# Optimization experiments

Hardware: AMD Instinct MI355X
Metric: run time of the kernel (lower is better)

## Reference

```python
import jax, jax.numpy as jnp
import numpy as np

N = 50000      # nodes
E = 500000     # edges per adjacency (avg degree ~10)
IN = 128       # in_dim == hidden_dim so layer weights stack cleanly
HID = 128
C = 40         # n_classes
L = 3          # n_layers
DEG = 10.0


def setup_inputs() -> dict:
    key = jax.random.key(0)
    ks = jax.random.split(key, 14)
    x0 = jax.random.normal(ks[0], (N, IN), jnp.float32)
    # COO sparse adjacency (row-sorted for efficient segment_sum); values mimic mean-normalized weights
    adj_row = jnp.sort(jax.random.randint(ks[1], (E,), 0, N, jnp.int32))
    adj_col = jax.random.randint(ks[2], (E,), 0, N, jnp.int32)
    adj_val = jax.random.uniform(ks[3], (E,), jnp.float32) / DEG
    adj_b_row = jnp.sort(jax.random.randint(ks[4], (E,), 0, N, jnp.int32))
    adj_b_col = jax.random.randint(ks[5], (E,), 0, N, jnp.int32)
    adj_b_val = jax.random.uniform(ks[6], (E,), jnp.float32) / DEG
    id_old_value_new = jax.random.randint(ks[7], (N,), 0, N, jnp.int32)
    mix_ratio = jnp.array([0.5], jnp.float32)
    s = 1.0 / np.sqrt(HID)
    # SAGEConv params: lin_l (applied to aggregated neighbors, carries bias) and lin_r (root)
    Wl = jax.random.uniform(ks[8], (L, HID, HID), jnp.float32, -s, s)
    Wr = jax.random.uniform(ks[9], (L, HID, HID), jnp.float32, -s, s)
    b_sage = jax.random.uniform(ks[10], (L, HID), jnp.float32, -s, s)
    so = 1.0 / np.sqrt(HID)
    W_out = jax.random.uniform(ks[11], (HID, C), jnp.float32, -so, so)
    b_out = jax.random.uniform(ks[12], (C,), jnp.float32, -so, so)
    return dict(x0=x0, adj_row=adj_row, adj_col=adj_col, adj_val=adj_val,
                adj_b_row=adj_b_row, adj_b_col=adj_b_col, adj_b_val=adj_b_val,
                mix_ratio=mix_ratio, id_old_value_new=id_old_value_new,
                Wl=Wl, Wr=Wr, b_sage=b_sage, W_out=W_out, b_out=b_out)


def _sage(x_src, x_dst, row, col, val, Wl_i, Wr_i, b_i):
    # spmm: aggr = adj @ x_src  (gather neighbor feats, scale by edge value, scatter-add to rows)
    msg = x_src[col] * val[:, None]                       # [E, HID]
    aggr = jax.ops.segment_sum(msg, row, num_segments=N)  # [N, HID]
    return aggr @ Wl_i + x_dst @ Wr_i + b_i


def reference(x0, adj_row, adj_col, adj_val, adj_b_row, adj_b_col, adj_b_val,
              mix_ratio, id_old_value_new, Wl, Wr, b_sage, W_out, b_out):
    r = mix_ratio
    # Branch A pre-aggregation stack (dropout is identity in eval mode)
    aggr_xs = [x0]
    x = x0
    for i in range(L - 1):
        x = jax.nn.relu(_sage(x, x, adj_row, adj_col, adj_val, Wl[i], Wr[i], b_sage[i]))
        aggr_xs.append(x)
    # Branch B: gather-based re-indexing of branch-A features
    aggr_xs_b = [h[id_old_value_new] for h in aggr_xs]
    x_mix = aggr_xs[0] * r + aggr_xs_b[0] * (1.0 - r)
    for i in range(L):
        x_new = jax.nn.relu(_sage(aggr_xs[i], x_mix, adj_row, adj_col, adj_val, Wl[i], Wr[i], b_sage[i]))
        x_new_b = jax.nn.relu(_sage(aggr_xs_b[i], x_mix, adj_b_row, adj_b_col, adj_b_val, Wl[i], Wr[i], b_sage[i]))
        x_mix = x_new * r + x_new_b * (1.0 - r)
    logits = x_mix @ W_out + b_out
    return jax.nn.log_softmax(logits, axis=-1)
```

## Files before the change

kernel.cpp:

```cpp
#include <hip/hip_runtime.h>
#include <hip/hip_fp16.h>
#include <math.h>

#define NNODES 50000
#define NEDGES 500000
#define HID 128
#define NCLS 40

using half8v = __attribute__((ext_vector_type(8))) _Float16;
using float4v = __attribute__((ext_vector_type(4))) float;
using uint4v = __attribute__((ext_vector_type(4))) unsigned;

static __device__ __forceinline__ unsigned h2u(__half2 h) {
    union { __half2 h; unsigned u; } x; x.h = h; return x.u;
}
static __device__ __forceinline__ __half2 u2h(unsigned u) {
    union { unsigned u; __half2 h; } x; x.u = u; return x.h;
}

static __device__ __forceinline__ void rowptr_body(const int* __restrict__ row,
                                                   int e, int* __restrict__ rp) {
    if (e >= NEDGES) return;
    int r = row[e];
    int prev = (e == 0) ? -1 : row[e - 1];
    for (int q = prev + 1; q <= r; ++q) rp[q] = e;
    if (e == NEDGES - 1) {
        for (int q = r + 1; q <= NNODES; ++q) rp[q] = NEDGES;
    }
}

static __global__ void prep_edges_kernel(const int* __restrict__ arow,
                                         const int* __restrict__ acol,
                                         const float* __restrict__ aval,
                                         const int* __restrict__ brow,
                                         const int* __restrict__ bcol,
                                         const float* __restrict__ bval,
                                         const int* __restrict__ id,
                                         int* __restrict__ rpa, int* __restrict__ rpb,
                                         int2* __restrict__ cvA, int2* __restrict__ cvB,
                                         int gE) {
    int bid = blockIdx.x;
    if (bid < gE) {
        rowptr_body(arow, bid * 256 + threadIdx.x, rpa);
    } else if (bid < 2 * gE) {
        rowptr_body(brow, (bid - gE) * 256 + threadIdx.x, rpb);
    } else if (bid < 3 * gE) {
        int e = (bid - 2 * gE) * 256 + threadIdx.x;
        if (e < NEDGES) {
            __half2 v = __float2half2_rn(aval[e]);
            cvA[e] = make_int2(acol[e], (int)h2u(v));
        }
    } else {
        int e = (bid - 3 * gE) * 256 + threadIdx.x;
        if (e < NEDGES) {
            __half2 v = __float2half2_rn(bval[e]);
            cvB[e] = make_int2(id[bcol[e]], (int)h2u(v));
        }
    }
}

static __global__ void prep_x_kernel(const float4* __restrict__ x, const int* __restrict__ id,
                                     const float* __restrict__ mixr,
                                     uint2* __restrict__ x0h, uint2* xmh) {
    int i = blockIdx.x * blockDim.x + threadIdx.x;
    int n = i >> 5, qq = i & 31;
    float r = mixr[0];
    float4 a = x[i];
    float4 b = x[(size_t)id[n] * 32 + qq];
    uint2 pa, pm;
    pa.x = h2u(__floats2half2_rn(a.x, a.y));
    pa.y = h2u(__floats2half2_rn(a.z, a.w));
    pm.x = h2u(__floats2half2_rn(r * a.x + (1.f - r) * b.x, r * a.y + (1.f - r) * b.y));
    pm.y = h2u(__floats2half2_rn(r * a.z + (1.f - r) * b.z, r * a.w + (1.f - r) * b.w));
    x0h[i] = pa;
    xmh[i] = pm;
}

static __global__ void prep_w_kernel(const float* __restrict__ Wl, const float* __restrict__ Wr,
                                     const float* __restrict__ Wout,
                                     __half* __restrict__ Wt, __half* __restrict__ WoT) {
    int t = blockIdx.x * blockDim.x + threadIdx.x;
    if (t < 6 * 16384) {
        int mat = t >> 14, idx = t & 16383;
        int n = idx >> 7, k = idx & 127;
        const float* src = (mat < 3) ? (Wl + mat * 16384) : (Wr + (mat - 3) * 16384);
        Wt[t] = __float2half(src[k * HID + n]);
    } else {
        int u = t - 6 * 16384;
        int c = u >> 7, k = u & 127;
        WoT[u] = (c < NCLS) ? __float2half(Wout[k * NCLS + c]) : __float2half(0.f);
    }
}

static __global__ __launch_bounds__(256, 8) void spmm2_kernel(
    const __half* __restrict__ h,
    const int2* __restrict__ cvA, const int* __restrict__ rpA,
    __half* __restrict__ Sh,
    const int2* __restrict__ cvB, const int* __restrict__ rpB,
    __half* __restrict__ Th) {
    int w = blockIdx.x * 4 + (threadIdx.x >> 6);
    const int l = threadIdx.x & 63;
    const int q = l >> 4, j = l & 15;
    const int2* cv; const int* rp; __half* dst; int node;
    if (w < NNODES) { cv = cvA; rp = rpA; dst = Sh; node = w; }
    else            { cv = cvB; rp = rpB; dst = Th; node = w - NNODES; }
    const int e0 = rp[node], e1 = rp[node + 1];
    __half2 a0 = __float2half2_rn(0.f), a1 = a0, a2 = a0, a3 = a0;
    int e = e0 + q;
    int2 m0, m1;
    bool have = (e + 4 < e1);
    if (have) { m0 = cv[e]; m1 = cv[e + 4]; }
    while (have) {
        const int e2 = e + 8;
        const bool nxt = (e2 + 4 < e1);
        int2 k0 = m0, k1 = m1;
        if (nxt) { k0 = cv[e2]; k1 = cv[e2 + 4]; }
        const uint4 p0 = *(const uint4*)(h + (size_t)m0.x * HID + j * 8);
        const uint4 p1 = *(const uint4*)(h + (size_t)m1.x * HID + j * 8);
        const __half2 v0 = u2h((unsigned)m0.y), v1 = u2h((unsigned)m1.y);
        a0 = __hfma2(u2h(p0.x), v0, a0); a1 = __hfma2(u2h(p0.y), v0, a1);
        a2 = __hfma2(u2h(p0.z), v0, a2); a3 = __hfma2(u2h(p0.w), v0, a3);
        a0 = __hfma2(u2h(p1.x), v1, a0); a1 = __hfma2(u2h(p1.y), v1, a1);
        a2 = __hfma2(u2h(p1.z), v1, a2); a3 = __hfma2(u2h(p1.w), v1, a3);
        m0 = k0; m1 = k1; e = e2; have = nxt;
    }
    if (e < e1) {
        const int2 m = cv[e];
        const uint4 p = *(const uint4*)(h + (size_t)m.x * HID + j * 8);
        const __half2 v = u2h((unsigned)m.y);
        a0 = __hfma2(u2h(p.x), v, a0); a1 = __hfma2(u2h(p.y), v, a1);
        a2 = __hfma2(u2h(p.z), v, a2); a3 = __hfma2(u2h(p.w), v, a3);
    }
    a0 = __hadd2(a0, u2h(__shfl_xor((int)h2u(a0), 16)));
    a1 = __hadd2(a1, u2h(__shfl_xor((int)h2u(a1), 16)));
    a2 = __hadd2(a2, u2h(__shfl_xor((int)h2u(a2), 16)));
    a3 = __hadd2(a3, u2h(__shfl_xor((int)h2u(a3), 16)));
    a0 = __hadd2(a0, u2h(__shfl_xor((int)h2u(a0), 32)));
    a1 = __hadd2(a1, u2h(__shfl_xor((int)h2u(a1), 32)));
    a2 = __hadd2(a2, u2h(__shfl_xor((int)h2u(a2), 32)));
    a3 = __hadd2(a3, u2h(__shfl_xor((int)h2u(a3), 32)));
    if (l < 16) {
        uint4v o;
        o.x = h2u(a0); o.y = h2u(a1); o.z = h2u(a2); o.w = h2u(a3);
        __builtin_nontemporal_store(o, (uint4v*)(dst + (size_t)node * HID + l * 8));
    }
}

#define LOAD_H4(ptr, w0, w1, w2, w3)                                            \
    w0 = *(const half8v*)(ptr);                                                 \
    w1 = *(const half8v*)((ptr) + 32);                                          \
    w2 = *(const half8v*)((ptr) + 64);                                          \
    w3 = *(const half8v*)((ptr) + 96);

#define LOAD_H4NT(ptr, w0, w1, w2, w3)                                          \
    w0 = __builtin_nontemporal_load((const half8v*)(ptr));                      \
    w1 = __builtin_nontemporal_load((const half8v*)((ptr) + 32));               \
    w2 = __builtin_nontemporal_load((const half8v*)((ptr) + 64));               \
    w3 = __builtin_nontemporal_load((const half8v*)((ptr) + 96));

#define MFMA4(w0, w1, w2, w3, x0, x1, x2, x3, t)                                \
    t = __builtin_amdgcn_mfma_f32_16x16x32_f16(w0, x0, t, 0, 0, 0);             \
    t = __builtin_amdgcn_mfma_f32_16x16x32_f16(w1, x1, t, 0, 0, 0);             \
    t = __builtin_amdgcn_mfma_f32_16x16x32_f16(w2, x2, t, 0, 0, 0);             \
    t = __builtin_amdgcn_mfma_f32_16x16x32_f16(w3, x3, t, 0, 0, 0);

template <bool DO_HY>
static __global__ __launch_bounds__(256, 4) void fused_layer_kernel(
    const __half* __restrict__ Sh, const __half* __restrict__ Th,
    __half* xm, const __half* __restrict__ hIn,
    const __half* __restrict__ Wl, const __half* __restrict__ Wr,
    const float* __restrict__ bias, const float* __restrict__ mixr,
    __half* __restrict__ hOut,
    const __half* __restrict__ WoT, const float* __restrict__ bout,
    float* __restrict__ out) {
    __shared__ __align__(16) _Float16 Wls[2][16][136];
    __shared__ __align__(16) _Float16 Wrs[2][16][136];
    __shared__ __align__(16) __half hs[DO_HY ? 1 : 64][136];
    const int tid = threadIdx.x;
    const int lr = tid & 15;
    const int lg = (tid >> 4) & 3;
    const int wv = tid >> 6;
    const int row = blockIdx.x * 64 + wv * 16 + lr;
    const int rowc = min(row, NNODES - 1);
    const size_t rbase = (size_t)rowc * HID;
    const float rr = mixr[0];
    const int srow = tid >> 4, scol = (tid & 15) * 8;

    half8v sh0, sh1, sh2, sh3, th0, th1, th2, th3;
    half8v xm0, xm1, xm2, xm3, hh0, hh1, hh2, hh3;
    {
        const __half* p = Sh + rbase + lg * 8;
        LOAD_H4NT(p, sh0, sh1, sh2, sh3)
        p = Th + rbase + lg * 8;
        LOAD_H4NT(p, th0, th1, th2, th3)
        p = xm + rbase + lg * 8;
        LOAD_H4(p, xm0, xm1, xm2, xm3)
        if constexpr (DO_HY) {
            p = hIn + rbase + lg * 8;
            LOAD_H4(p, hh0, hh1, hh2, hh3)
        }
    }

    half8v wlreg = *(const half8v*)(Wl + srow * HID + scol);
    half8v wrreg = *(const half8v*)(Wr + srow * HID + scol);

#pragma unroll
    for (int c = 0; c < 8; ++c) {
        const int buf = c & 1;
        *(half8v*)&Wls[buf][srow][scol] = wlreg;
        *(half8v*)&Wrs[buf][srow][scol] = wrreg;
        if (c < 7) {
            wlreg = *(const half8v*)(Wl + (c + 1) * 2048 + srow * HID + scol);
            wrreg = *(const half8v*)(Wr + (c + 1) * 2048 + srow * HID + scol);
        }
        __syncthreads();

        const _Float16* wlp = &Wls[buf][lr][lg * 8];
        const _Float16* wrp = &Wrs[buf][lr][lg * 8];
        half8v l0, l1, l2, l3, r0, r1, r2, r3;
        LOAD_H4(wlp, l0, l1, l2, l3)
        LOAD_H4(wrp, r0, r1, r2, r3)
        float4v aS = {0.f, 0.f, 0.f, 0.f}, aT = aS, aZ = aS, aH = aS;
        MFMA4(l0, l1, l2, l3, sh0, sh1, sh2, sh3, aS)
        MFMA4(l0, l1, l2, l3, th0, th1, th2, th3, aT)
        MFMA4(r0, r1, r2, r3, xm0, xm1, xm2, xm3, aZ)
        if constexpr (DO_HY) {
            MFMA4(r0, r1, r2, r3, hh0, hh1, hh2, hh3, aH)
        }
        const int col0 = c * 16 + lg * 4;
        const float4v bv = *(const float4v*)(bias + col0);
        __half xm4[4], h4[4];
#pragma unroll
        for (int i = 0; i < 4; ++i) {
            const float z = aZ[i] + bv[i];
            const float xa = fmaxf(aS[i] + z, 0.f);
            const float xb = fmaxf(aT[i] + z, 0.f);
            xm4[i] = __float2half(rr * xa + (1.f - rr) * xb);
            if constexpr (DO_HY) h4[i] = __float2half(fmaxf(aS[i] + aH[i] + bv[i], 0.f));
        }
        uint2 xmv;
        xmv.x = h2u(__half2{xm4[0], xm4[1]});
        xmv.y = h2u(__half2{xm4[2], xm4[3]});
        if constexpr (DO_HY) {
            uint2 hv;
            hv.x = h2u(__half2{h4[0], h4[1]});
            hv.y = h2u(__half2{h4[2], h4[3]});
            if (row < NNODES) {
                *(uint2*)(xm + rbase + col0) = xmv;
                *(uint2*)(hOut + rbase + col0) = hv;
            }
        } else {
            *(uint2*)(&hs[wv * 16 + lr][col0]) = xmv;
        }
        __syncthreads();
    }

    if constexpr (!DO_HY) {
        const __half* lp = &hs[wv * 16 + lr][lg * 8];
        half8v c0, c1, c2, c3;
        LOAD_H4(lp, c0, c1, c2, c3)
        float lv[3][4];
        float mx = -INFINITY;
#pragma unroll
        for (int c = 0; c < 3; ++c) {
            const __half* wq = WoT + (size_t)(c * 16 + lr) * HID + lg * 8;
            half8v w0, w1, w2, w3;
            LOAD_H4(wq, w0, w1, w2, w3)
            float4v t = {0.f, 0.f, 0.f, 0.f};
            MFMA4(w0, w1, w2, w3, c0, c1, c2, c3, t)
            const int col0 = c * 16 + lg * 4;
            const bool valid = col0 < NCLS;
#pragma unroll
            for (int i = 0; i < 4; ++i) {
                const float l = valid ? (t[i] + bout[col0 + i]) : -INFINITY;
                lv[c][i] = l;
                mx = fmaxf(mx, l);
            }
        }
        mx = fmaxf(mx, __shfl_xor(mx, 16));
        mx = fmaxf(mx, __shfl_xor(mx, 32));
        float sum = 0.f;
#pragma unroll
        for (int c = 0; c < 3; ++c)
#pragma unroll
            for (int i = 0; i < 4; ++i)
                if (lv[c][i] > -INFINITY) sum += expf(lv[c][i] - mx);
        sum += __shfl_xor(sum, 16);
        sum += __shfl_xor(sum, 32);
        const float lse = mx + logf(sum);
#pragma unroll
        for (int c = 0; c < 3; ++c) {
            const int col0 = c * 16 + lg * 4;
            if (col0 < NCLS && row < NNODES) {
                float4 o = make_float4(lv[c][0] - lse, lv[c][1] - lse,
                                       lv[c][2] - lse, lv[c][3] - lse);
                *(float4*)(out + (size_t)row * NCLS + col0) = o;
            }
        }
    }
}

extern "C" void kernel_launch(void* const* d_in, const int* in_sizes, int n_in,
                              void* d_out, int out_size, void* d_ws, size_t ws_size,
                              hipStream_t stream) {
    const float* x0   = (const float*)d_in[0];
    const int*   arow = (const int*)d_in[1];
    const int*   acol = (const int*)d_in[2];
    const float* aval = (const float*)d_in[3];
    const int*   brow = (const int*)d_in[4];
    const int*   bcol = (const int*)d_in[5];
    const float* bval = (const float*)d_in[6];
    const float* mixr = (const float*)d_in[7];
    const int*   id   = (const int*)d_in[8];
    const float* Wl   = (const float*)d_in[9];
    const float* Wr   = (const float*)d_in[10];
    const float* bs   = (const float*)d_in[11];
    const float* Wout = (const float*)d_in[12];
    const float* bout = (const float*)d_in[13];
    float* out = (float*)d_out;

    const size_t NF = (size_t)NNODES * HID;
    __half* x0h = (__half*)d_ws;
    __half* xmh = x0h + NF;
    __half* h1  = xmh + NF;
    __half* h2  = h1 + NF;
    __half* Sh  = h2 + NF;
    __half* Th  = Sh + NF;
    __half* Wt  = Th + NF;
    __half* WoT = Wt + 6 * 16384;
    int2* cvA = (int2*)(WoT + 48 * 128);
    int2* cvB = cvA + NEDGES;
    int* rpa = (int*)(cvB + NEDGES);
    int* rpb = rpa + (NNODES + 1);

    const int gE = (NEDGES + 255) / 256;
    const int gC = NNODES * HID / 4 / 256;
    const int gG = (NNODES + 63) / 64;
    const int gS2 = 2 * NNODES * 64 / 256;

    prep_edges_kernel<<<4 * gE, 256, 0, stream>>>(arow, acol, aval, brow, bcol, bval,
                                                  id, rpa, rpb, cvA, cvB, gE);
    prep_x_kernel<<<gC, 256, 0, stream>>>((const float4*)x0, id, mixr,
                                          (uint2*)x0h, (uint2*)xmh);
    prep_w_kernel<<<(6 * 16384 + 48 * 128) / 256, 256, 0, stream>>>(Wl, Wr, Wout, Wt, WoT);

    spmm2_kernel<<<gS2, 256, 0, stream>>>(x0h, cvA, rpa, Sh, cvB, rpb, Th);
    fused_layer_kernel<true><<<gG, 256, 0, stream>>>(
        Sh, Th, xmh, x0h, Wt + 0 * 16384, Wt + 3 * 16384, bs, mixr,
        h1, nullptr, nullptr, nullptr);

    spmm2_kernel<<<gS2, 256, 0, stream>>>(h1, cvA, rpa, Sh, cvB, rpb, Th);
    fused_layer_kernel<true><<<gG, 256, 0, stream>>>(
        Sh, Th, xmh, h1, Wt + 1 * 16384, Wt + 4 * 16384, bs + 128, mixr,
        h2, nullptr, nullptr, nullptr);

    spmm2_kernel<<<gS2, 256, 0, stream>>>(h2, cvA, rpa, Sh, cvB, rpb, Th);
    fused_layer_kernel<false><<<gG, 256, 0, stream>>>(
        Sh, Th, xmh, nullptr, Wt + 2 * 16384, Wt + 5 * 16384, bs + 256, mixr,
        nullptr, WoT, bout, out);
}
```

Before: 216.1 us.

## Fuse SpMM aggregation into layer kernel via shared-memory staging

Removes the separate spmm2 kernel and computes both adjacency aggregations inside the layer kernel, staging each block's 64 rows of S and T in shared memory before the MFMA transform. This avoids writing and re-reading the two N×128 half intermediates and drops a launch per layer. In exchange, each 16-lane group now walks the A and B edge lists for 4 nodes serially with one edge per step, so there is less memory-level parallelism than the old 4-way edge split. Occupancy also drops because of the larger LDS use and the lower launch bound.

After: 320.0 us. +48.1%, slower.

```diff
diff --git a/kernel.cpp b/kernel.cpp
--- a/kernel.cpp
+++ b/kernel.cpp
@@ -92,72 +92,12 @@
     }
 }
 
-static __global__ __launch_bounds__(256, 8) void spmm2_kernel(
-    const __half* __restrict__ h,
-    const int2* __restrict__ cvA, const int* __restrict__ rpA,
-    __half* __restrict__ Sh,
-    const int2* __restrict__ cvB, const int* __restrict__ rpB,
-    __half* __restrict__ Th) {
-    int w = blockIdx.x * 4 + (threadIdx.x >> 6);
-    const int l = threadIdx.x & 63;
-    const int q = l >> 4, j = l & 15;
-    const int2* cv; const int* rp; __half* dst; int node;
-    if (w < NNODES) { cv = cvA; rp = rpA; dst = Sh; node = w; }
-    else            { cv = cvB; rp = rpB; dst = Th; node = w - NNODES; }
-    const int e0 = rp[node], e1 = rp[node + 1];
-    __half2 a0 = __float2half2_rn(0.f), a1 = a0, a2 = a0, a3 = a0;
-    int e = e0 + q;
-    int2 m0, m1;
-    bool have = (e + 4 < e1);
-    if (have) { m0 = cv[e]; m1 = cv[e + 4]; }
-    while (have) {
-        const int e2 = e + 8;
-        const bool nxt = (e2 + 4 < e1);
-        int2 k0 = m0, k1 = m1;
-        if (nxt) { k0 = cv[e2]; k1 = cv[e2 + 4]; }
-        const uint4 p0 = *(const uint4*)(h + (size_t)m0.x * HID + j * 8);
-        const uint4 p1 = *(const uint4*)(h + (size_t)m1.x * HID + j * 8);
-        const __half2 v0 = u2h((unsigned)m0.y), v1 = u2h((unsigned)m1.y);
-        a0 = __hfma2(u2h(p0.x), v0, a0); a1 = __hfma2(u2h(p0.y), v0, a1);
-        a2 = __hfma2(u2h(p0.z), v0, a2); a3 = __hfma2(u2h(p0.w), v0, a3);
-        a0 = __hfma2(u2h(p1.x), v1, a0); a1 = __hfma2(u2h(p1.y), v1, a1);
-        a2 = __hfma2(u2h(p1.z), v1, a2); a3 = __hfma2(u2h(p1.w), v1, a3);
-        m0 = k0; m1 = k1; e = e2; have = nxt;
-    }
-    if (e < e1) {
-        const int2 m = cv[e];
-        const uint4 p = *(const uint4*)(h + (size_t)m.x * HID + j * 8);
-        const __half2 v = u2h((unsigned)m.y);
-        a0 = __hfma2(u2h(p.x), v, a0); a1 = __hfma2(u2h(p.y), v, a1);
-        a2 = __hfma2(u2h(p.z), v, a2); a3 = __hfma2(u2h(p.w), v, a3);
-    }
-    a0 = __hadd2(a0, u2h(__shfl_xor((int)h2u(a0), 16)));
-    a1 = __hadd2(a1, u2h(__shfl_xor((int)h2u(a1), 16)));
-    a2 = __hadd2(a2, u2h(__shfl_xor((int)h2u(a2), 16)));
-    a3 = __hadd2(a3, u2h(__shfl_xor((int)h2u(a3), 16)));
-    a0 = __hadd2(a0, u2h(__shfl_xor((int)h2u(a0), 32)));
-    a1 = __hadd2(a1, u2h(__shfl_xor((int)h2u(a1), 32)));
-    a2 = __hadd2(a2, u2h(__shfl_xor((int)h2u(a2), 32)));
-    a3 = __hadd2(a3, u2h(__shfl_xor((int)h2u(a3), 32)));
-    if (l < 16) {
-        uint4v o;
-        o.x = h2u(a0); o.y = h2u(a1); o.z = h2u(a2); o.w = h2u(a3);
-        __builtin_nontemporal_store(o, (uint4v*)(dst + (size_t)node * HID + l * 8));
-    }
-}
-
 #define LOAD_H4(ptr, w0, w1, w2, w3)                                            \
     w0 = *(const half8v*)(ptr);                                                 \
     w1 = *(const half8v*)((ptr) + 32);                                          \
     w2 = *(const half8v*)((ptr) + 64);                                          \
     w3 = *(const half8v*)((ptr) + 96);
 
-#define LOAD_H4NT(ptr, w0, w1, w2, w3)                                          \
-    w0 = __builtin_nontemporal_load((const half8v*)(ptr));                      \
-    w1 = __builtin_nontemporal_load((const half8v*)((ptr) + 32));               \
-    w2 = __builtin_nontemporal_load((const half8v*)((ptr) + 64));               \
-    w3 = __builtin_nontemporal_load((const half8v*)((ptr) + 96));
-
 #define MFMA4(w0, w1, w2, w3, x0, x1, x2, x3, t)                                \
     t = __builtin_amdgcn_mfma_f32_16x16x32_f16(w0, x0, t, 0, 0, 0);             \
     t = __builtin_amdgcn_mfma_f32_16x16x32_f16(w1, x1, t, 0, 0, 0);             \
@@ -165,44 +105,94 @@
     t = __builtin_amdgcn_mfma_f32_16x16x32_f16(w3, x3, t, 0, 0, 0);
 
 template <bool DO_HY>
-static __global__ __launch_bounds__(256, 4) void fused_layer_kernel(
-    const __half* __restrict__ Sh, const __half* __restrict__ Th,
-    __half* xm, const __half* __restrict__ hIn,
+static __global__ __launch_bounds__(256, 3) void layer_kernel(
+    const __half* __restrict__ src,
+    const int2* __restrict__ cvA, const int* __restrict__ rpA,
+    const int2* __restrict__ cvB, const int* __restrict__ rpB,
+    __half* xm,
     const __half* __restrict__ Wl, const __half* __restrict__ Wr,
     const float* __restrict__ bias, const float* __restrict__ mixr,
     __half* __restrict__ hOut,
     const __half* __restrict__ WoT, const float* __restrict__ bout,
     float* __restrict__ out) {
+    __shared__ __align__(16) _Float16 Sls[64][136];
+    __shared__ __align__(16) _Float16 Tls[64][136];
     __shared__ __align__(16) _Float16 Wls[2][16][136];
     __shared__ __align__(16) _Float16 Wrs[2][16][136];
-    __shared__ __align__(16) __half hs[DO_HY ? 1 : 64][136];
     const int tid = threadIdx.x;
     const int lr = tid & 15;
     const int lg = (tid >> 4) & 3;
     const int wv = tid >> 6;
-    const int row = blockIdx.x * 64 + wv * 16 + lr;
+    const int gr0 = blockIdx.x * 64;
+    const int row = gr0 + wv * 16 + lr;
     const int rowc = min(row, NNODES - 1);
     const size_t rbase = (size_t)rowc * HID;
     const float rr = mixr[0];
     const int srow = tid >> 4, scol = (tid & 15) * 8;
 
-    half8v sh0, sh1, sh2, sh3, th0, th1, th2, th3;
     half8v xm0, xm1, xm2, xm3, hh0, hh1, hh2, hh3;
     {
-        const __half* p = Sh + rbase + lg * 8;
-        LOAD_H4NT(p, sh0, sh1, sh2, sh3)
-        p = Th + rbase + lg * 8;
-        LOAD_H4NT(p, th0, th1, th2, th3)
-        p = xm + rbase + lg * 8;
+        const __half* p = xm + rbase + lg * 8;
         LOAD_H4(p, xm0, xm1, xm2, xm3)
         if constexpr (DO_HY) {
-            p = hIn + rbase + lg * 8;
+            p = src + rbase + lg * 8;
             LOAD_H4(p, hh0, hh1, hh2, hh3)
         }
     }
-
-    half8v wlreg = *(const half8v*)(Wl + srow * HID + scol);
-    half8v wrreg = *(const half8v*)(Wr + srow * HID + scol);
+    half8v wlreg = *(const half8v*)((const _Float16*)Wl + srow * HID + scol);
+    half8v wrreg = *(const half8v*)((const _Float16*)Wr + srow * HID + scol);
+
+    {
+        const int qw = tid >> 4;
+        const int j = tid & 15;
+        const __half2 hz = __float2half2_rn(0.f);
+#pragma unroll
+        for (int k = 0; k < 4; ++k) {
+            const int nl = qw * 4 + k;
+            const int node = gr0 + nl;
+            __half2 sa0 = hz, sa1 = hz, sa2 = hz, sa3 = hz;
+            __half2 ta0 = hz, ta1 = hz, ta2 = hz, ta3 = hz;
+            if (node < NNODES) {
+                int eA = rpA[node];
+                const int aE = rpA[node + 1];
+                int eB = rpB[node];
+                const int bE = rpB[node + 1];
+                int2 mA = cvA[min(eA, NEDGES - 1)];
+                int2 mB = cvB[min(eB, NEDGES - 1)];
+                while (eA < aE || eB < bE) {
+                    const bool vA = eA < aE, vB = eB < bE;
+                    const int eA2 = eA + (vA ? 1 : 0);
+                    const int eB2 = eB + (vB ? 1 : 0);
+                    const int2 nA = cvA[min(eA2, NEDGES - 1)];
+                    const int2 nB = cvB[min(eB2, NEDGES - 1)];
+                    const uint4 pA = *(const uint4*)(src + (size_t)mA.x * HID + j * 8);
+                    const uint4 pB = *(const uint4*)(src + (size_t)mB.x * HID + j * 8);
+                    const __half2 vvA = vA ? u2h((unsigned)mA.y) : hz;
+                    const __half2 vvB = vB ? u2h((unsigned)mB.y) : hz;
+                    sa0 = __hfma2(u2h(pA.x), vvA, sa0); sa1 = __hfma2(u2h(pA.y), vvA, sa1);
+                    sa2 = __hfma2(u2h(pA.z), vvA, sa2); sa3 = __hfma2(u2h(pA.w), vvA, sa3);
+                    ta0 = __hfma2(u2h(pB.x), vvB, ta0); ta1 = __hfma2(u2h(pB.y), vvB, ta1);
+                    ta2 = __hfma2(u2h(pB.z), vvB, ta2); ta3 = __hfma2(u2h(pB.w), vvB, ta3);
+                    mA = nA; mB = nB; eA = eA2; eB = eB2;
+                }
+            }
+            uint4v os, ot;
+            os.x = h2u(sa0); os.y = h2u(sa1); os.z = h2u(sa2); os.w = h2u(sa3);
+            ot.x = h2u(ta0); ot.y = h2u(ta1); ot.z = h2u(ta2); ot.w = h2u(ta3);
+            *(uint4v*)&Sls[nl][j * 8] = os;
+            *(uint4v*)&Tls[nl][j * 8] = ot;
+        }
+    }
+    __syncthreads();
+
+    half8v sh0, sh1, sh2, sh3, th0, th1, th2, th3;
+    {
+        const _Float16* sp = &Sls[wv * 16 + lr][lg * 8];
+        LOAD_H4(sp, sh0, sh1, sh2, sh3)
+        const _Float16* tp = &Tls[wv * 16 + lr][lg * 8];
+        LOAD_H4(tp, th0, th1, th2, th3)
+    }
+    _Float16 (*hs)[136] = Sls;
 
 #pragma unroll
     for (int c = 0; c < 8; ++c) {
@@ -210,8 +200,8 @@
         *(half8v*)&Wls[buf][srow][scol] = wlreg;
         *(half8v*)&Wrs[buf][srow][scol] = wrreg;
         if (c < 7) {
-            wlreg = *(const half8v*)(Wl + (c + 1) * 2048 + srow * HID + scol);
-            wrreg = *(const half8v*)(Wr + (c + 1) * 2048 + srow * HID + scol);
+            wlreg = *(const half8v*)((const _Float16*)Wl + (c + 1) * 2048 + srow * HID + scol);
+            wrreg = *(const half8v*)((const _Float16*)Wr + (c + 1) * 2048 + srow * HID + scol);
         }
         __syncthreads();
 
@@ -250,13 +240,13 @@
                 *(uint2*)(hOut + rbase + col0) = hv;
             }
         } else {
-            *(uint2*)(&hs[wv * 16 + lr][col0]) = xmv;
+            *(uint2*)((__half*)&hs[wv * 16 + lr][col0]) = xmv;
         }
         __syncthreads();
     }
 
     if constexpr (!DO_HY) {
-        const __half* lp = &hs[wv * 16 + lr][lg * 8];
+        const _Float16* lp = &hs[wv * 16 + lr][lg * 8];
         half8v c0, c1, c2, c3;
         LOAD_H4(lp, c0, c1, c2, c3)
         float lv[3][4];
@@ -324,9 +314,7 @@
     __half* xmh = x0h + NF;
     __half* h1  = xmh + NF;
     __half* h2  = h1 + NF;
-    __half* Sh  = h2 + NF;
-    __half* Th  = Sh + NF;
-    __half* Wt  = Th + NF;
+    __half* Wt  = h2 + NF;
     __half* WoT = Wt + 6 * 16384;
     int2* cvA = (int2*)(WoT + 48 * 128);
     int2* cvB = cvA + NEDGES;
@@ -336,7 +324,6 @@
     const int gE = (NEDGES + 255) / 256;
     const int gC = NNODES * HID / 4 / 256;
     const int gG = (NNODES + 63) / 64;
-    const int gS2 = 2 * NNODES * 64 / 256;
 
     prep_edges_kernel<<<4 * gE, 256, 0, stream>>>(arow, acol, aval, brow, bcol, bval,
                                                   id, rpa, rpb, cvA, cvB, gE);
@@ -344,18 +331,18 @@
                                           (uint2*)x0h, (uint2*)xmh);
     prep_w_kernel<<<(6 * 16384 + 48 * 128) / 256, 256, 0, stream>>>(Wl, Wr, Wout, Wt, WoT);
 
-    spmm2_kernel<<<gS2, 256, 0, stream>>>(x0h, cvA, rpa, Sh, cvB, rpb, Th);
-    fused_layer_kernel<true><<<gG, 256, 0, stream>>>(
-        Sh, Th, xmh, x0h, Wt + 0 * 16384, Wt + 3 * 16384, bs, mixr,
+    layer_kernel<true><<<gG, 256, 0, stream>>>(
+        x0h, cvA, rpa, cvB, rpb, xmh,
+        Wt + 0 * 16384, Wt + 3 * 16384, bs, mixr,
         h1, nullptr, nullptr, nullptr);
 
-    spmm2_kernel<<<gS2, 256, 0, stream>>>(h1, cvA, rpa, Sh, cvB, rpb, Th);
-    fused_layer_kernel<true><<<gG, 256, 0, stream>>>(
-        Sh, Th, xmh, h1, Wt + 1 * 16384, Wt + 4 * 16384, bs + 128, mixr,
+    layer_kernel<true><<<gG, 256, 0, stream>>>(
+        h1, cvA, rpa, cvB, rpb, xmh,
+        Wt + 1 * 16384, Wt + 4 * 16384, bs + 128, mixr,
         h2, nullptr, nullptr, nullptr);
 
-    spmm2_kernel<<<gS2, 256, 0, stream>>>(h2, cvA, rpa, Sh, cvB, rpb, Th);
-    fused_layer_kernel<false><<<gG, 256, 0, stream>>>(
-        Sh, Th, xmh, nullptr, Wt + 2 * 16384, Wt + 5 * 16384, bs + 256, mixr,
+    layer_kernel<false><<<gG, 256, 0, stream>>>(
+        h2, cvA, rpa, cvB, rpb, xmh,
+        Wt + 2 * 16384, Wt + 5 * 16384, bs + 256, mixr,
         nullptr, WoT, bout, out);
 }
```
